# Kernel tuning notes

Measured on AMD Instinct MI355X. Metric: run time of the kernel, lower is better.

## Reference

```python
import jax, jax.numpy as jnp
import numpy as np
from jax import lax

STD_H, STD_W = 364, 280
RADIUS, SIGMA = 15, 4.0


def gaussian_kernel():
    r = jnp.arange(-RADIUS, RADIUS + 1, dtype=jnp.float32)
    d2 = r[:, None] ** 2 + r[None, :] ** 2
    k = jnp.exp(-0.5 / (SIGMA ** 2) * d2)
    k = k / k.sum()
    return k[None, None]  # (1,1,31,31) OIHW


def setup_inputs() -> dict:
    key = jax.random.key(0)
    k1, k2 = jax.random.split(key)
    B, H, W = 32, 512, 512
    input_face = jax.random.uniform(k1, (B, 3, H, W), dtype=jnp.float32)
    # landmarks in (x, y) pixel coords within the HxW image
    landmarks = jax.random.uniform(k2, (B, 68, 2), dtype=jnp.float32) * jnp.array([W, H], jnp.float32)
    weight = gaussian_kernel()
    return {"input_face": input_face, "landmarks": landmarks, "weight": weight}


def _blur(x, weight):
    # x: (B,1,h,w), 31x31 'same' conv (kernel symmetric, so corr == conv)
    return lax.conv_general_dilated(x, weight, (1, 1), 'SAME',
                                    dimension_numbers=('NCHW', 'OIHW', 'NCHW'))


def reference(input_face, landmarks, weight):
    B, C, H, W = input_face.shape
    scaling = STD_H / H
    lm = landmarks * scaling                      # (B,68,2) in standard coords
    center = lm[:, 30:31, :]                      # (B,1,2)

    p0 = lm[:, 30:36, :]
    p1 = lm[:, 2:15, :]
    p2 = lm[:, 48:68, :]
    p3 = lm[:, 6:11, :]
    p01 = (p0 - center) * 1.5 + center
    p11 = (p1 - center) * 0.5 + center
    p12 = (p1 - center) * 0.7 + center
    p13 = (p1 - center) * 0.9 + center
    p21 = (p2 - center) * 1.3 + center
    keys = jnp.concatenate([p0, p01, p12, p13, p11, p2, p3, p21], axis=-2)  # (B,96,2)

    iy = jnp.round(jnp.clip(keys[..., 1], 0, STD_H - 1)).astype(jnp.int32)
    ix = jnp.round(jnp.clip(keys[..., 0], 0, STD_W - 1)).astype(jnp.int32)

    # Faithful to torch advanced-indexing semantics: union of ALL batches'
    # points is written into every batch's heatmap.
    hm = jnp.zeros((STD_H, STD_W), jnp.float32).at[iy.ravel(), ix.ravel()].set(1.0)
    hm = jnp.broadcast_to(hm[None, None], (B, 1, STD_H, STD_W))

    w1 = _blur(hm, weight)
    w2 = jnp.where(w1 > 1e-7, 1.0, w1)
    w3 = _blur(w2, weight)

    w_mask = jax.image.resize(w3, (B, 1, H, W), method='bilinear')
    return (1.0 - w_mask) * input_face  # filling='black'
```

## Files before the change

### kernel.cpp

```cpp
#include <hip/hip_runtime.h>

#define BB   32
#define HH   512
#define WW   512
#define SH   364
#define SW   280
#define RAD  15
#define NK   96
#define OMN  (HH*WW)
#define PF4  (OMN/4)

#define OH   16
#define OW   32
#define NRM  13
#define NCM  19
#define WRM  (NRM + 2*RAD)
#define HRM  (NRM + 4*RAD)
#define HCP  84
#define WCP  52
#define NCP  20
#define G1   13
#define G2   5

typedef float f4 __attribute__((ext_vector_type(4)));

__device__ __forceinline__ void point_ij(const float* __restrict__ lm, int b, int j,
                                         int& ix, int& iy) {
    int idx; float s;
    if      (j <  6) { idx = 30 + j;        s = 1.0f; }
    else if (j < 12) { idx = 30 + (j - 6);  s = 1.5f; }
    else if (j < 25) { idx =  2 + (j - 12); s = 0.7f; }
    else if (j < 38) { idx =  2 + (j - 25); s = 0.9f; }
    else if (j < 51) { idx =  2 + (j - 38); s = 0.5f; }
    else if (j < 71) { idx = 48 + (j - 51); s = 1.0f; }
    else if (j < 76) { idx =  6 + (j - 71); s = 1.0f; }
    else             { idx = 48 + (j - 76); s = 1.3f; }
    const float scal = 364.0f / 512.0f;
    float lx = lm[b * 136 + idx * 2 + 0] * scal;
    float ly = lm[b * 136 + idx * 2 + 1] * scal;
    float kx, ky;
    if (s == 1.0f) { kx = lx; ky = ly; }
    else {
        float cx = lm[b * 136 + 30 * 2 + 0] * scal;
        float cy = lm[b * 136 + 30 * 2 + 1] * scal;
        kx = (lx - cx) * s + cx;
        ky = (ly - cy) * s + cy;
    }
    ix = __float2int_rn(fminf(fmaxf(kx, 0.0f), (float)(SW - 1)));
    iy = __float2int_rn(fminf(fmaxf(ky, 0.0f), (float)(SH - 1)));
}

__global__ __launch_bounds__(256) void k_mask(const float* __restrict__ lm,
                                              const float* __restrict__ wt,
                                              float* __restrict__ om) {
    __shared__ float gwl[31];
    __shared__ alignas(16) float hmS[HRM][HCP];
    __shared__ alignas(16) float t1 [HRM][WCP];
    __shared__ alignas(16) float w2S[WRM][WCP];
    __shared__ alignas(16) float t2 [WRM][NCP];
    __shared__ alignas(16) float w3S[NRM][NCP];

    const int tid = threadIdx.x;
    const int h0 = blockIdx.y * OH, w0 = blockIdx.x * OW;
    const float sy = (float)SH / (float)HH;
    const float sx = (float)SW / (float)WW;

    if (tid < 31) gwl[tid] = wt[15 * 31 + tid] / sqrtf(wt[15 * 31 + 15]);

    const int hl = h0 + OH - 1, wl = w0 + OW - 1;
    float fy0 = fmaxf(((float)h0 + 0.5f) * sy - 0.5f, 0.0f);
    float fyl = fminf(((float)hl + 0.5f) * sy - 0.5f, (float)(SH - 1));
    int rbase = (int)fy0;
    int rend  = min(SH - 1, (int)fyl + 1);
    float fx0 = fmaxf(((float)w0 + 0.5f) * sx - 0.5f, 0.0f);
    float fxl = fminf(((float)wl + 0.5f) * sx - 0.5f, (float)(SW - 1));
    int cbase = (int)fx0;
    int cend  = min(SW - 1, (int)fxl + 1);
    int NR = rend - rbase + 1;
    int NC = cend - cbase + 1;
    int HR = NR + 4 * RAD, HC = NC + 4 * RAD;

    for (int i = tid; i < HRM * HCP; i += 256) ((float*)hmS)[i] = 0.0f;
    __syncthreads();

    float g[31];
    #pragma unroll
    for (int k = 0; k < 31; ++k) g[k] = gwl[k];

    for (int p = tid; p < BB * NK; p += 256) {
        int b = p / NK, j = p - b * NK;
        int ix, iy;
        point_ij(lm, b, j, ix, iy);
        int ly = iy - (rbase - 2 * RAD), lx = ix - (cbase - 2 * RAD);
        if (ly >= 0 && ly < HR && lx >= 0 && lx < HC) hmS[ly][lx] = 1.0f;
    }
    __syncthreads();

    for (int it = tid; it < HRM * G1; it += 256) {
        int y = it / G1, c0 = (it - y * G1) * 4;
        float r[34];
        #pragma unroll
        for (int k = 0; k < 34; ++k) r[k] = hmS[y][c0 + k];
        #pragma unroll
        for (int q = 0; q < 4; ++q) {
            float acc = 0.0f;
            #pragma unroll
            for (int d = 0; d < 31; ++d) acc += g[d] * r[q + d];
            t1[y][c0 + q] = acc;
        }
    }
    __syncthreads();

    for (int it = tid; it < WRM * G1; it += 256) {
        int y = it / G1, c0 = (it - y * G1) * 4;
        f4 acc = {0.0f, 0.0f, 0.0f, 0.0f};
        #pragma unroll
        for (int d = 0; d < 31; ++d) {
            f4 v = *(const f4*)&t1[y + d][c0];
            acc += v * g[d];
        }
        int gy = rbase - RAD + y;
        bool rowok = (gy >= 0 && gy < SH);
        #pragma unroll
        for (int q = 0; q < 4; ++q) {
            float v = acc[q];
            v = (v > 1e-7f) ? 1.0f : v;
            int gx = cbase - RAD + c0 + q;
            w2S[y][c0 + q] = (rowok && gx >= 0 && gx < SW) ? v : 0.0f;
        }
    }
    __syncthreads();

    for (int it = tid; it < WRM * G2; it += 256) {
        int y = it / G2, c0 = (it - y * G2) * 4;
        float r[34];
        #pragma unroll
        for (int k = 0; k < 34; ++k) r[k] = w2S[y][c0 + k];
        #pragma unroll
        for (int q = 0; q < 4; ++q) {
            float acc = 0.0f;
            #pragma unroll
            for (int d = 0; d < 31; ++d) acc += g[d] * r[q + d];
            t2[y][c0 + q] = acc;
        }
    }
    __syncthreads();

    for (int it = tid; it < NRM * G2; it += 256) {
        int y = it / G2, c0 = (it - y * G2) * 4;
        f4 acc = {0.0f, 0.0f, 0.0f, 0.0f};
        #pragma unroll
        for (int d = 0; d < 31; ++d) {
            f4 v = *(const f4*)&t2[y + d][c0];
            acc += v * g[d];
        }
        *(f4*)&w3S[y][c0] = acc;
    }
    __syncthreads();

    for (int i = tid; i < OH * OW; i += 256) {
        int dh = i / OW, dw = i - dh * OW;
        int h = h0 + dh, w = w0 + dw;
        float fy = fminf(fmaxf(((float)h + 0.5f) * sy - 0.5f, 0.0f), (float)(SH - 1));
        float fx = fminf(fmaxf(((float)w + 0.5f) * sx - 0.5f, 0.0f), (float)(SW - 1));
        int y0 = (int)fy, x0 = (int)fx;
        int y1 = min(y0 + 1, SH - 1), x1 = min(x0 + 1, SW - 1);
        float ty = fy - (float)y0, tx = fx - (float)x0;
        int ly0 = y0 - rbase, ly1 = y1 - rbase;
        int lx0 = x0 - cbase, lx1 = x1 - cbase;
        float v00 = w3S[ly0][lx0], v01 = w3S[ly0][lx1];
        float v10 = w3S[ly1][lx0], v11 = w3S[ly1][lx1];
        float v = (1.0f - ty) * ((1.0f - tx) * v00 + tx * v01)
                +         ty  * ((1.0f - tx) * v10 + tx * v11);
        om[h * WW + w] = 1.0f - v;
    }
}

__global__ __launch_bounds__(256) void k_final(const f4* __restrict__ in,
                                               const f4* __restrict__ om,
                                               f4* __restrict__ out) {
    const int pg    = blockIdx.x >> 8;
    const int chunk = blockIdx.x & 255;
    const int ofs   = (chunk << 8) + threadIdx.x;
    const long b0   = (long)(pg * 4) * PF4 + ofs;
    f4 m  = om[ofs];
    f4 a0 = in[b0];
    f4 a1 = in[b0 + PF4];
    f4 a2 = in[b0 + 2 * PF4];
    f4 a3 = in[b0 + 3 * PF4];
    __builtin_nontemporal_store(a0 * m, &out[b0]);
    __builtin_nontemporal_store(a1 * m, &out[b0 + PF4]);
    __builtin_nontemporal_store(a2 * m, &out[b0 + 2 * PF4]);
    __builtin_nontemporal_store(a3 * m, &out[b0 + 3 * PF4]);
}

extern "C" void kernel_launch(void* const* d_in, const int* in_sizes, int n_in,
                              void* d_out, int out_size, void* d_ws, size_t ws_size,
                              hipStream_t stream) {
    const float* face = (const float*)d_in[0];
    const float* lm   = (const float*)d_in[1];
    const float* wt   = (const float*)d_in[2];

    float* om = (float*)d_ws;

    k_mask<<<dim3(WW / OW, HH / OH), 256, 0, stream>>>(lm, wt, om);
    k_final<<<6144, 256, 0, stream>>>(
        (const f4*)face, (const f4*)om, (f4*)d_out);
}
```

Before: 52.56 us.

## Fuse mask computation and face multiply into one kernel

```diff
diff --git a/kernel.cpp b/kernel.cpp
--- a/kernel.cpp
+++ b/kernel.cpp
@@ -50,15 +50,17 @@
     iy = __float2int_rn(fminf(fmaxf(ky, 0.0f), (float)(SH - 1)));
 }
 
-__global__ __launch_bounds__(256) void k_mask(const float* __restrict__ lm,
-                                              const float* __restrict__ wt,
-                                              float* __restrict__ om) {
+__global__ __launch_bounds__(256) void k_fused(const float* __restrict__ lm,
+                                               const float* __restrict__ wt,
+                                               const f4* __restrict__ face,
+                                               f4* __restrict__ out) {
     __shared__ float gwl[31];
     __shared__ alignas(16) float hmS[HRM][HCP];
     __shared__ alignas(16) float t1 [HRM][WCP];
     __shared__ alignas(16) float w2S[WRM][WCP];
     __shared__ alignas(16) float t2 [WRM][NCP];
     __shared__ alignas(16) float w3S[NRM][NCP];
+    __shared__ alignas(16) float maskS[OH][OW];
 
     const int tid = threadIdx.x;
     const int h0 = blockIdx.y * OH, w0 = blockIdx.x * OW;
@@ -172,26 +174,21 @@
         float v10 = w3S[ly1][lx0], v11 = w3S[ly1][lx1];
         float v = (1.0f - ty) * ((1.0f - tx) * v00 + tx * v01)
                 +         ty  * ((1.0f - tx) * v10 + tx * v11);
-        om[h * WW + w] = 1.0f - v;
-    }
-}
-
-__global__ __launch_bounds__(256) void k_final(const f4* __restrict__ in,
-                                               const f4* __restrict__ om,
-                                               f4* __restrict__ out) {
-    const int pg    = blockIdx.x >> 8;
-    const int chunk = blockIdx.x & 255;
-    const int ofs   = (chunk << 8) + threadIdx.x;
-    const long b0   = (long)(pg * 4) * PF4 + ofs;
-    f4 m  = om[ofs];
-    f4 a0 = in[b0];
-    f4 a1 = in[b0 + PF4];
-    f4 a2 = in[b0 + 2 * PF4];
-    f4 a3 = in[b0 + 3 * PF4];
-    __builtin_nontemporal_store(a0 * m, &out[b0]);
-    __builtin_nontemporal_store(a1 * m, &out[b0 + PF4]);
-    __builtin_nontemporal_store(a2 * m, &out[b0 + 2 * PF4]);
-    __builtin_nontemporal_store(a3 * m, &out[b0 + 3 * PF4]);
+        maskS[dh][dw] = 1.0f - v;
+    }
+    __syncthreads();
+
+    const int j   = tid & 127;
+    const int grp = tid >> 7;
+    const int dh  = j >> 3, dw4 = (j & 7) << 2;
+    const f4 m = *(const f4*)&maskS[dh][dw4];
+    const long off = (long)(h0 + dh) * (WW / 4) + ((w0 + dw4) >> 2);
+    #pragma unroll 8
+    for (int k = 0; k < 48; ++k) {
+        long idx = (long)(grp + 2 * k) * PF4 + off;
+        f4 a = face[idx];
+        __builtin_nontemporal_store(a * m, &out[idx]);
+    }
 }
 
 extern "C" void kernel_launch(void* const* d_in, const int* in_sizes, int n_in,
@@ -201,9 +198,6 @@
     const float* lm   = (const float*)d_in[1];
     const float* wt   = (const float*)d_in[2];
 
-    float* om = (float*)d_ws;
-
-    k_mask<<<dim3(WW / OW, HH / OH), 256, 0, stream>>>(lm, wt, om);
-    k_final<<<6144, 256, 0, stream>>>(
-        (const f4*)face, (const f4*)om, (f4*)d_out);
+    k_fused<<<dim3(WW / OW, HH / OH), 256, 0, stream>>>(
+        lm, wt, (const f4*)face, (f4*)d_out);
 }
```

Result: no change. 51.78 us (-1.5%).
